# Optimization experiments

Hardware: AMD Instinct MI355X
Metric: run time of the kernel (lower is better)

## Reference

```python
import jax, jax.numpy as jnp
import numpy as np
from jax.scipy.linalg import cho_solve

D, A, H, N, T = 64, 8, 256, 16, 128
DT = 0.05
# GPR hyperparameters set_hyperparameter(0.1, 0.1, 0.1): lengthscale, signal std, noise std
L2, SF2, SN2 = 0.1 ** 2, 0.1 ** 2, 0.1 ** 2


def _rbf(t1, t2):
    # t1: (P,), t2: (Q,) -> (P, Q) squared-exponential kernel
    d2 = (t1[:, None] - t2[None, :]) ** 2
    return SF2 * jnp.exp(-0.5 * d2 / L2)


def _gp_predict(t, y, tq):
    # t, y: (N,) training inputs/targets; tq: (T,) query times
    K = _rbf(t, t) + SN2 * jnp.eye(t.shape[0], dtype=t.dtype)
    Ks = _rbf(tq, t)          # (T, N)
    Kss = _rbf(tq, tq)        # (T, T)
    Lc = jnp.linalg.cholesky(K)
    alpha = cho_solve((Lc, True), y)        # (N,)
    V = cho_solve((Lc, True), Ks.T)         # (N, T)
    mu = Ks @ alpha                          # (T,)
    cov = Kss - Ks @ V                       # (T, T)
    return mu, cov


def setup_inputs() -> dict:
    key = jax.random.key(0)
    ks = jax.random.split(key, 8)
    def lin(k, out_d, in_d):
        return (jax.random.normal(k, (out_d, in_d), jnp.float32) / np.sqrt(in_d).astype(np.float32))
    return {
        "x": jax.random.normal(ks[0], (512, D), jnp.float32),
        "a": jax.random.normal(ks[1], (512, A), jnp.float32),
        "da": jax.random.normal(ks[2], (512, A), jnp.float32),
        "W1": lin(ks[3], H, D), "b1": jnp.zeros((H,), jnp.float32),
        "W2": lin(ks[4], H, H), "b2": jnp.zeros((H,), jnp.float32),
        "Wt": lin(ks[5], N, H), "bt": jnp.zeros((N,), jnp.float32),
        "Wa": lin(ks[6], N * A, H), "ba": jnp.zeros((N * A,), jnp.float32),
        "time_array": jnp.arange(1, T + 1, dtype=jnp.float32) * DT,
    }


def reference(x, a, da, W1, b1, W2, b2, Wt, bt, Wa, ba, time_array):
    E = x.shape[0]
    h = jnp.tanh(x @ W1.T + b1)
    h = jnp.tanh(h @ W2.T + b2)
    times = h @ Wt.T + bt                              # (E, N)
    anchors = (h @ Wa.T + ba).reshape(E, A, N)         # (E, A, N)
    ts = jnp.broadcast_to(times[:, None, :], (E, A, N)).reshape(E * A, N)
    ys = anchors.reshape(E * A, N)
    mu, cov = jax.vmap(lambda t, y: _gp_predict(t, y, time_array))(ts, ys)
    return mu.reshape(E, A, T), cov.reshape(E, A, T, T)
```

## Files before the change

### kernel.cpp

```cpp
#include <hip/hip_runtime.h>

#define Ecnt 512
#define Dd 64
#define Aa 8
#define Hh 256
#define Nn 16
#define Tt 128
#define NH 144
#define SF2c 0.01f
#define SN2c 0.01f
#define NEGHALF_INV_L2 (-50.0f)

#define OFF_W1T 0
#define OFF_W2T (OFF_W1T + Dd * Hh)
#define OFF_WHT (OFF_W2T + Hh * Hh)
#define OFF_BH  (OFF_WHT + Hh * NH)
#define OFF_TT  (OFF_BH + NH)
#define OFF_KS  (OFF_TT + Ecnt * Nn)
#define OFF_V   (OFF_KS + Ecnt * Tt * Nn)
#define WS_FLOATS (OFF_V + Ecnt * Nn * Tt)

__global__ void prep(const float* __restrict__ W1, const float* __restrict__ W2,
                     const float* __restrict__ Wt, const float* __restrict__ Wa,
                     const float* __restrict__ bt, const float* __restrict__ ba,
                     float* __restrict__ ws) {
    int id = blockIdx.x * blockDim.x + threadIdx.x;
    if (id < Dd * Hh) {
        int k = id >> 8, o = id & 255;
        ws[OFF_W1T + id] = W1[o * Dd + k];
    } else if (id < OFF_WHT) {
        int r = id - OFF_W2T; int k = r >> 8, o = r & 255;
        ws[id] = W2[o * Hh + k];
    } else if (id < OFF_BH) {
        int r = id - OFF_WHT; int k = r / NH, j = r % NH;
        ws[id] = (j < Nn) ? Wt[j * Hh + k] : Wa[(j - Nn) * Hh + k];
    } else if (id < OFF_TT) {
        int j = id - OFF_BH;
        ws[id] = (j < Nn) ? bt[j] : ba[j - Nn];
    }
}

__global__ __launch_bounds__(256, 2) void grp_solve(
    const float* __restrict__ x,
    const float* __restrict__ b1, const float* __restrict__ b2,
    const float* __restrict__ tarr, float* __restrict__ ws,
    float* __restrict__ out_mu)
{
    const int e   = blockIdx.x;
    const int tid = threadIdx.x;

    __shared__ float xs[Dd];
    __shared__ float h1s[Hh];
    __shared__ float h2s[Hh];
    __shared__ float tt[Nn];
    __shared__ float tq[Tt];
    __shared__ float yy[Aa][Nn];
    __shared__ float Km[Nn][Nn + 1];
    __shared__ float Lm[Nn][Nn + 1];
    __shared__ float tmpv[Nn];
    __shared__ __align__(16) float Ks[Tt][Nn];
    __shared__ __align__(16) float V[Nn][Tt];
    __shared__ float alpha[Aa][Nn];

    if (tid < Dd) xs[tid] = x[e * Dd + tid];
    if (tid < Tt) tq[tid] = tarr[tid];
    __syncthreads();

    const float* __restrict__ W1T = ws + OFF_W1T;
    const float* __restrict__ W2T = ws + OFF_W2T;
    const float* __restrict__ WHT = ws + OFF_WHT;
    const float* __restrict__ BH  = ws + OFF_BH;

    {
        float acc = b1[tid];
        #pragma unroll 8
        for (int k = 0; k < Dd; ++k) acc += W1T[k * Hh + tid] * xs[k];
        h1s[tid] = tanhf(acc);
    }
    __syncthreads();
    {
        float acc = b2[tid];
        #pragma unroll 8
        for (int k = 0; k < Hh; ++k) acc += W2T[k * Hh + tid] * h1s[k];
        h2s[tid] = tanhf(acc);
    }
    __syncthreads();
    if (tid < NH) {
        float acc = BH[tid];
        #pragma unroll 8
        for (int k = 0; k < Hh; ++k) acc += WHT[k * NH + tid] * h2s[k];
        if (tid < Nn) tt[tid] = acc;
        else { int r = tid - Nn; yy[r >> 4][r & 15] = acc; }
    }
    __syncthreads();

    {
        int i = tid >> 4, j = tid & 15;
        float d = tt[i] - tt[j];
        Km[i][j] = SF2c * __expf(NEGHALF_INV_L2 * d * d) + (i == j ? SN2c : 0.f);
    }
    #pragma unroll
    for (int r = 0; r < 8; ++r) {
        int idx = tid + r * 256;
        int q = idx >> 4, i = idx & 15;
        float d = tq[q] - tt[i];
        Ks[q][i] = SF2c * __expf(NEGHALF_INV_L2 * d * d);
    }
    __syncthreads();

    for (int j = 0; j < Nn; ++j) {
        if (tid >= j && tid < Nn) {
            float s = Km[tid][j];
            for (int k = 0; k < j; ++k) s -= Lm[tid][k] * Lm[j][k];
            tmpv[tid] = s;
        }
        __syncthreads();
        if (tid >= j && tid < Nn) {
            float dj = sqrtf(tmpv[j]);
            Lm[tid][j] = (tid == j) ? dj : tmpv[tid] / dj;
        }
        __syncthreads();
    }

    if (tid < Tt + Aa) {
        float bz[Nn];
        if (tid < Tt) {
            float tqv = tq[tid];
            #pragma unroll
            for (int i = 0; i < Nn; ++i) {
                float d = tqv - tt[i];
                bz[i] = SF2c * __expf(NEGHALF_INV_L2 * d * d);
            }
        } else {
            int a = tid - Tt;
            #pragma unroll
            for (int i = 0; i < Nn; ++i) bz[i] = yy[a][i];
        }
        #pragma unroll
        for (int i = 0; i < Nn; ++i) {
            float s = bz[i];
            for (int k = 0; k < i; ++k) s -= Lm[i][k] * bz[k];
            bz[i] = s / Lm[i][i];
        }
        #pragma unroll
        for (int i = Nn - 1; i >= 0; --i) {
            float s = bz[i];
            for (int k = i + 1; k < Nn; ++k) s -= Lm[k][i] * bz[k];
            bz[i] = s / Lm[i][i];
        }
        if (tid < Tt) {
            #pragma unroll
            for (int i = 0; i < Nn; ++i) V[i][tid] = bz[i];
        } else {
            int a = tid - Tt;
            #pragma unroll
            for (int i = 0; i < Nn; ++i) alpha[a][i] = bz[i];
        }
    }
    __syncthreads();

    if (tid < Tt) {
        float ks[Nn];
        #pragma unroll
        for (int i = 0; i < Nn; ++i) ks[i] = Ks[tid][i];
        size_t mb = (size_t)e * (Aa * Tt) + tid;
        #pragma unroll
        for (int a = 0; a < Aa; ++a) {
            float m = 0.f;
            #pragma unroll
            for (int i = 0; i < Nn; ++i) m += ks[i] * alpha[a][i];
            out_mu[mb + (size_t)a * Tt] = m;
        }
    }

    if (tid < Nn) ws[OFF_TT + e * Nn + tid] = tt[tid];
    {
        float4* dK = (float4*)(ws + OFF_KS + (size_t)e * (Tt * Nn));
        const float4* sK = (const float4*)&Ks[0][0];
        dK[tid] = sK[tid];
        dK[tid + 256] = sK[tid + 256];
        float4* dV = (float4*)(ws + OFF_V + (size_t)e * (Nn * Tt));
        const float4* sV = (const float4*)&V[0][0];
        dV[tid] = sV[tid];
        dV[tid + 256] = sV[tid + 256];
    }
}

__global__ __launch_bounds__(256, 4) void grp_cov(
    const float* __restrict__ ws, const float* __restrict__ tarr,
    float* __restrict__ out_cov)
{
    const int b  = blockIdx.x;
    const int e  = b >> 2;
    const int ch = b & 3;
    const int tid = threadIdx.x;

    __shared__ __align__(16) float Vs[Nn][Tt];
    __shared__ __align__(16) float Ksl[32][Nn];
    __shared__ float tqs[Tt];

    {
        const float4* sV = (const float4*)(ws + OFF_V + (size_t)e * (Nn * Tt));
        float4* dV = (float4*)&Vs[0][0];
        dV[tid] = sV[tid];
        dV[tid + 256] = sV[tid + 256];
        if (tid < 128) {
            const float4* sK = (const float4*)(ws + OFF_KS + (size_t)e * (Tt * Nn) + (size_t)ch * 32 * Nn);
            ((float4*)&Ksl[0][0])[tid] = sK[tid];
        }
        if (tid < Tt) tqs[tid] = tarr[tid];
    }
    __syncthreads();

    const int q4 = (tid & 31) * 4;
    const int pr = tid >> 5;
    float vq[Nn][4];
    #pragma unroll
    for (int i = 0; i < Nn; ++i) {
        float4 vv = *(const float4*)&Vs[i][q4];
        vq[i][0] = vv.x; vq[i][1] = vv.y; vq[i][2] = vv.z; vq[i][3] = vv.w;
    }
    const float tqq0 = tqs[q4 + 0], tqq1 = tqs[q4 + 1], tqq2 = tqs[q4 + 2], tqq3 = tqs[q4 + 3];
    float* covb = out_cov + (size_t)e * (Aa * Tt * Tt);

    #pragma unroll
    for (int pp = 0; pp < 4; ++pp) {
        const int lp = pr * 4 + pp;
        const int p  = ch * 32 + lp;
        const float tqp = tqs[p];
        float d0 = tqp - tqq0, d1 = tqp - tqq1, d2 = tqp - tqq2, d3 = tqp - tqq3;
        float a0 = SF2c * __expf(NEGHALF_INV_L2 * d0 * d0);
        float a1 = SF2c * __expf(NEGHALF_INV_L2 * d1 * d1);
        float a2 = SF2c * __expf(NEGHALF_INV_L2 * d2 * d2);
        float a3 = SF2c * __expf(NEGHALF_INV_L2 * d3 * d3);
        #pragma unroll
        for (int i = 0; i < Nn; ++i) {
            float ks = Ksl[lp][i];
            a0 -= ks * vq[i][0];
            a1 -= ks * vq[i][1];
            a2 -= ks * vq[i][2];
            a3 -= ks * vq[i][3];
        }
        float4 pk; pk.x = a0; pk.y = a1; pk.z = a2; pk.w = a3;
        const size_t ro = (size_t)p * Tt + q4;
        #pragma unroll
        for (int a = 0; a < Aa; ++a) {
            *(float4*)(covb + (size_t)a * (Tt * Tt) + ro) = pk;
        }
    }
}

extern "C" void kernel_launch(void* const* d_in, const int* in_sizes, int n_in,
                              void* d_out, int out_size, void* d_ws, size_t ws_size,
                              hipStream_t stream) {
    (void)in_sizes; (void)n_in; (void)out_size; (void)ws_size;
    const float* x  = (const float*)d_in[0];
    const float* W1 = (const float*)d_in[3];
    const float* b1 = (const float*)d_in[4];
    const float* W2 = (const float*)d_in[5];
    const float* b2 = (const float*)d_in[6];
    const float* Wt = (const float*)d_in[7];
    const float* bt = (const float*)d_in[8];
    const float* Wa = (const float*)d_in[9];
    const float* ba = (const float*)d_in[10];
    const float* ta = (const float*)d_in[11];
    float* mu  = (float*)d_out;
    float* cov = mu + (size_t)Ecnt * Aa * Tt;
    float* wsf = (float*)d_ws;

    prep<<<(OFF_TT + 255) / 256, 256, 0, stream>>>(W1, W2, Wt, Wa, bt, ba, wsf);
    grp_solve<<<Ecnt, 256, 0, stream>>>(x, b1, b2, ta, wsf, mu);
    grp_cov<<<Ecnt * 4, 256, 0, stream>>>(wsf, ta, cov);
}
```

Before: 323.3 us.

## Rewrite GP solve kernel as a single wavefront using register shuffles

```diff
diff --git a/kernel.cpp b/kernel.cpp
--- a/kernel.cpp
+++ b/kernel.cpp
@@ -40,149 +40,170 @@
     }
 }
 
-__global__ __launch_bounds__(256, 2) void grp_solve(
+__global__ __launch_bounds__(64, 1) void grp_solve_wave(
     const float* __restrict__ x,
     const float* __restrict__ b1, const float* __restrict__ b2,
     const float* __restrict__ tarr, float* __restrict__ ws,
     float* __restrict__ out_mu)
 {
-    const int e   = blockIdx.x;
-    const int tid = threadIdx.x;
-
-    __shared__ float xs[Dd];
-    __shared__ float h1s[Hh];
-    __shared__ float h2s[Hh];
-    __shared__ float tt[Nn];
-    __shared__ float tq[Tt];
-    __shared__ float yy[Aa][Nn];
-    __shared__ float Km[Nn][Nn + 1];
-    __shared__ float Lm[Nn][Nn + 1];
-    __shared__ float tmpv[Nn];
-    __shared__ __align__(16) float Ks[Tt][Nn];
-    __shared__ __align__(16) float V[Nn][Tt];
-    __shared__ float alpha[Aa][Nn];
-
-    if (tid < Dd) xs[tid] = x[e * Dd + tid];
-    if (tid < Tt) tq[tid] = tarr[tid];
-    __syncthreads();
-
-    const float* __restrict__ W1T = ws + OFF_W1T;
-    const float* __restrict__ W2T = ws + OFF_W2T;
-    const float* __restrict__ WHT = ws + OFF_WHT;
-    const float* __restrict__ BH  = ws + OFF_BH;
-
-    {
-        float acc = b1[tid];
-        #pragma unroll 8
-        for (int k = 0; k < Dd; ++k) acc += W1T[k * Hh + tid] * xs[k];
-        h1s[tid] = tanhf(acc);
-    }
-    __syncthreads();
-    {
-        float acc = b2[tid];
-        #pragma unroll 8
-        for (int k = 0; k < Hh; ++k) acc += W2T[k * Hh + tid] * h1s[k];
-        h2s[tid] = tanhf(acc);
-    }
-    __syncthreads();
-    if (tid < NH) {
-        float acc = BH[tid];
-        #pragma unroll 8
-        for (int k = 0; k < Hh; ++k) acc += WHT[k * NH + tid] * h2s[k];
-        if (tid < Nn) tt[tid] = acc;
-        else { int r = tid - Nn; yy[r >> 4][r & 15] = acc; }
-    }
-    __syncthreads();
-
-    {
-        int i = tid >> 4, j = tid & 15;
-        float d = tt[i] - tt[j];
-        Km[i][j] = SF2c * __expf(NEGHALF_INV_L2 * d * d) + (i == j ? SN2c : 0.f);
-    }
-    #pragma unroll
-    for (int r = 0; r < 8; ++r) {
-        int idx = tid + r * 256;
-        int q = idx >> 4, i = idx & 15;
-        float d = tq[q] - tt[i];
-        Ks[q][i] = SF2c * __expf(NEGHALF_INV_L2 * d * d);
-    }
-    __syncthreads();
-
-    for (int j = 0; j < Nn; ++j) {
-        if (tid >= j && tid < Nn) {
-            float s = Km[tid][j];
-            for (int k = 0; k < j; ++k) s -= Lm[tid][k] * Lm[j][k];
-            tmpv[tid] = s;
-        }
-        __syncthreads();
-        if (tid >= j && tid < Nn) {
-            float dj = sqrtf(tmpv[j]);
-            Lm[tid][j] = (tid == j) ? dj : tmpv[tid] / dj;
-        }
-        __syncthreads();
-    }
-
-    if (tid < Tt + Aa) {
-        float bz[Nn];
-        if (tid < Tt) {
-            float tqv = tq[tid];
-            #pragma unroll
-            for (int i = 0; i < Nn; ++i) {
-                float d = tqv - tt[i];
-                bz[i] = SF2c * __expf(NEGHALF_INV_L2 * d * d);
-            }
-        } else {
-            int a = tid - Tt;
-            #pragma unroll
-            for (int i = 0; i < Nn; ++i) bz[i] = yy[a][i];
-        }
-        #pragma unroll
-        for (int i = 0; i < Nn; ++i) {
-            float s = bz[i];
-            for (int k = 0; k < i; ++k) s -= Lm[i][k] * bz[k];
-            bz[i] = s / Lm[i][i];
-        }
-        #pragma unroll
-        for (int i = Nn - 1; i >= 0; --i) {
-            float s = bz[i];
-            for (int k = i + 1; k < Nn; ++k) s -= Lm[k][i] * bz[k];
-            bz[i] = s / Lm[i][i];
-        }
-        if (tid < Tt) {
-            #pragma unroll
-            for (int i = 0; i < Nn; ++i) V[i][tid] = bz[i];
-        } else {
-            int a = tid - Tt;
-            #pragma unroll
-            for (int i = 0; i < Nn; ++i) alpha[a][i] = bz[i];
-        }
-    }
-    __syncthreads();
-
-    if (tid < Tt) {
-        float ks[Nn];
-        #pragma unroll
-        for (int i = 0; i < Nn; ++i) ks[i] = Ks[tid][i];
-        size_t mb = (size_t)e * (Aa * Tt) + tid;
-        #pragma unroll
-        for (int a = 0; a < Aa; ++a) {
-            float m = 0.f;
-            #pragma unroll
-            for (int i = 0; i < Nn; ++i) m += ks[i] * alpha[a][i];
-            out_mu[mb + (size_t)a * Tt] = m;
-        }
-    }
-
-    if (tid < Nn) ws[OFF_TT + e * Nn + tid] = tt[tid];
-    {
-        float4* dK = (float4*)(ws + OFF_KS + (size_t)e * (Tt * Nn));
-        const float4* sK = (const float4*)&Ks[0][0];
-        dK[tid] = sK[tid];
-        dK[tid + 256] = sK[tid + 256];
-        float4* dV = (float4*)(ws + OFF_V + (size_t)e * (Nn * Tt));
-        const float4* sV = (const float4*)&V[0][0];
-        dV[tid] = sV[tid];
-        dV[tid + 256] = sV[tid + 256];
+    const int e = blockIdx.x;
+    const int l = threadIdx.x;
+
+    const float4* __restrict__ W1T4 = (const float4*)(ws + OFF_W1T);
+    const float4* __restrict__ W2T4 = (const float4*)(ws + OFF_W2T);
+    const float4* __restrict__ WHT4 = (const float4*)(ws + OFF_WHT);
+    const float*  __restrict__ BH   = ws + OFF_BH;
+
+    const float xreg = x[e * Dd + l];
+    const float2 tq2 = *(const float2*)&tarr[2 * l];
+
+    float4 bv = *(const float4*)&b1[4 * l];
+    float a0 = bv.x, a1 = bv.y, a2 = bv.z, a3 = bv.w;
+    #pragma unroll 8
+    for (int k = 0; k < Dd; ++k) {
+        float hk = __shfl(xreg, k);
+        float4 w = W1T4[k * 64 + l];
+        a0 += w.x * hk; a1 += w.y * hk; a2 += w.z * hk; a3 += w.w * hk;
+    }
+    float h0 = tanhf(a0), h1 = tanhf(a1), h2 = tanhf(a2), h3 = tanhf(a3);
+
+    bv = *(const float4*)&b2[4 * l];
+    a0 = bv.x; a1 = bv.y; a2 = bv.z; a3 = bv.w;
+    #pragma unroll 4
+    for (int k0 = 0; k0 < 64; ++k0) {
+        float g0 = __shfl(h0, k0), g1 = __shfl(h1, k0);
+        float g2 = __shfl(h2, k0), g3 = __shfl(h3, k0);
+        float4 w;
+        w = W2T4[(4 * k0 + 0) * 64 + l]; a0 += w.x * g0; a1 += w.y * g0; a2 += w.z * g0; a3 += w.w * g0;
+        w = W2T4[(4 * k0 + 1) * 64 + l]; a0 += w.x * g1; a1 += w.y * g1; a2 += w.z * g1; a3 += w.w * g1;
+        w = W2T4[(4 * k0 + 2) * 64 + l]; a0 += w.x * g2; a1 += w.y * g2; a2 += w.z * g2; a3 += w.w * g2;
+        w = W2T4[(4 * k0 + 3) * 64 + l]; a0 += w.x * g3; a1 += w.y * g3; a2 += w.z * g3; a3 += w.w * g3;
+    }
+    h0 = tanhf(a0); h1 = tanhf(a1); h2 = tanhf(a2); h3 = tanhf(a3);
+
+    float c0 = 0.f, c1 = 0.f, c2 = 0.f, c3 = 0.f;
+    if (l < 36) {
+        float4 bh = *(const float4*)&BH[4 * l];
+        c0 = bh.x; c1 = bh.y; c2 = bh.z; c3 = bh.w;
+    }
+    #pragma unroll 4
+    for (int k0 = 0; k0 < 64; ++k0) {
+        float g0 = __shfl(h0, k0), g1 = __shfl(h1, k0);
+        float g2 = __shfl(h2, k0), g3 = __shfl(h3, k0);
+        if (l < 36) {
+            float4 w;
+            w = WHT4[(4 * k0 + 0) * 36 + l]; c0 += w.x * g0; c1 += w.y * g0; c2 += w.z * g0; c3 += w.w * g0;
+            w = WHT4[(4 * k0 + 1) * 36 + l]; c0 += w.x * g1; c1 += w.y * g1; c2 += w.z * g1; c3 += w.w * g1;
+            w = WHT4[(4 * k0 + 2) * 36 + l]; c0 += w.x * g2; c1 += w.y * g2; c2 += w.z * g2; c3 += w.w * g2;
+            w = WHT4[(4 * k0 + 3) * 36 + l]; c0 += w.x * g3; c1 += w.y * g3; c2 += w.z * g3; c3 += w.w * g3;
+        }
+    }
+
+    float ttv[16];
+    #pragma unroll
+    for (int i = 0; i < 16; ++i) {
+        float src = ((i & 3) == 0) ? c0 : ((i & 3) == 1) ? c1 : ((i & 3) == 2) ? c2 : c3;
+        ttv[i] = __shfl(src, i >> 2);
+    }
+    float z2[16];
+    #pragma unroll
+    for (int i = 0; i < 16; ++i) {
+        int src = (4 + 4 * (l - 48) + (i >> 2)) & 63;
+        float v = ((i & 3) == 0) ? c0 : ((i & 3) == 1) ? c1 : ((i & 3) == 2) ? c2 : c3;
+        z2[i] = __shfl(v, src);
+    }
+
+    float tsel = ttv[0];
+    #pragma unroll
+    for (int i = 1; i < 16; ++i) tsel = (l == i) ? ttv[i] : tsel;
+    float Krow[16];
+    #pragma unroll
+    for (int j = 0; j < 16; ++j) {
+        float d = tsel - ttv[j];
+        Krow[j] = SF2c * __expf(NEGHALF_INV_L2 * d * d) + ((l == j) ? SN2c : 0.f);
+    }
+
+    float Lrow[16];
+    #pragma unroll
+    for (int j = 0; j < 16; ++j) {
+        float s = Krow[j];
+        #pragma unroll
+        for (int k = 0; k < j; ++k) {
+            float Ljk = __shfl(Lrow[k], j);
+            s -= Lrow[k] * Ljk;
+        }
+        float dj = __shfl(s, j);
+        float dsq = sqrtf(dj);
+        float rinv = 1.0f / dsq;
+        Lrow[j] = (l == j) ? dsq : s * rinv;
+    }
+
+    float Ksr0[16], Ksr1[16];
+    #pragma unroll
+    for (int i = 0; i < 16; ++i) {
+        float d0 = tq2.x - ttv[i];
+        float d1 = tq2.y - ttv[i];
+        Ksr0[i] = SF2c * __expf(NEGHALF_INV_L2 * d0 * d0);
+        Ksr1[i] = SF2c * __expf(NEGHALF_INV_L2 * d1 * d1);
+    }
+    float z0[16], z1[16];
+    #pragma unroll
+    for (int i = 0; i < 16; ++i) { z0[i] = Ksr0[i]; z1[i] = Ksr1[i]; }
+
+    #pragma unroll
+    for (int i = 0; i < 16; ++i) {
+        #pragma unroll
+        for (int k = 0; k < i; ++k) {
+            float Lik = __shfl(Lrow[k], i);
+            z0[i] -= Lik * z0[k];
+            z1[i] -= Lik * z1[k];
+            z2[i] -= Lik * z2[k];
+        }
+        float Lii = __shfl(Lrow[i], i);
+        float r = 1.0f / Lii;
+        z0[i] *= r; z1[i] *= r; z2[i] *= r;
+    }
+    #pragma unroll
+    for (int i = 15; i >= 0; --i) {
+        #pragma unroll
+        for (int k = i + 1; k < 16; ++k) {
+            float Lki = __shfl(Lrow[i], k);
+            z0[i] -= Lki * z0[k];
+            z1[i] -= Lki * z1[k];
+            z2[i] -= Lki * z2[k];
+        }
+        float Lii = __shfl(Lrow[i], i);
+        float r = 1.0f / Lii;
+        z0[i] *= r; z1[i] *= r; z2[i] *= r;
+    }
+
+    float* __restrict__ wsV = ws + OFF_V + (size_t)e * (Nn * Tt);
+    #pragma unroll
+    for (int i = 0; i < 16; ++i) {
+        float2 p; p.x = z0[i]; p.y = z1[i];
+        *(float2*)&wsV[i * Tt + 2 * l] = p;
+    }
+    float* __restrict__ wsK = ws + OFF_KS + (size_t)e * (Tt * Nn);
+    #pragma unroll
+    for (int m = 0; m < 4; ++m) {
+        float4 p0; p0.x = Ksr0[4*m+0]; p0.y = Ksr0[4*m+1]; p0.z = Ksr0[4*m+2]; p0.w = Ksr0[4*m+3];
+        *(float4*)&wsK[(2 * l) * Nn + 4 * m] = p0;
+        float4 p1; p1.x = Ksr1[4*m+0]; p1.y = Ksr1[4*m+1]; p1.z = Ksr1[4*m+2]; p1.w = Ksr1[4*m+3];
+        *(float4*)&wsK[(2 * l + 1) * Nn + 4 * m] = p1;
+    }
+
+    float* __restrict__ mub = out_mu + (size_t)e * (Aa * Tt);
+    #pragma unroll
+    for (int a = 0; a < Aa; ++a) {
+        float m0 = 0.f, m1 = 0.f;
+        #pragma unroll
+        for (int i = 0; i < 16; ++i) {
+            float al = __shfl(z2[i], 48 + a);
+            m0 += Ksr0[i] * al;
+            m1 += Ksr1[i] * al;
+        }
+        float2 p; p.x = m0; p.y = m1;
+        *(float2*)&mub[a * Tt + 2 * l] = p;
     }
 }
 
@@ -269,6 +290,6 @@
     float* wsf = (float*)d_ws;
 
     prep<<<(OFF_TT + 255) / 256, 256, 0, stream>>>(W1, W2, Wt, Wa, bt, ba, wsf);
-    grp_solve<<<Ecnt, 256, 0, stream>>>(x, b1, b2, ta, wsf, mu);
+    grp_solve_wave<<<Ecnt, 64, 0, stream>>>(x, b1, b2, ta, wsf, mu);
     grp_cov<<<Ecnt * 4, 256, 0, stream>>>(wsf, ta, cov);
 }
```

After: 334.5 us. 3.5% more time.
